# Kernel optimization log

Hardware: AMD Instinct MI355X
Metric: run time of the kernel (lower is better)

## Reference

```python
import jax, jax.numpy as jnp
import numpy as np

DIM = 2048
DIM_HEAD = 64
HEADS = 16
FF_MULT = 4
ATTN_INNER = DIM_HEAD * HEADS          # 1024
FF_INNER = DIM * FF_MULT               # 8192
FUSED = ATTN_INNER + DIM_HEAD + DIM_HEAD + FF_INNER  # 9344
EPS = 1e-8


def setup_inputs() -> dict:
    key = jax.random.key(0)
    ks = jax.random.split(key, 8)
    b, n = 2, 2048
    x = jax.random.normal(ks[0], (b, n, DIM), dtype=jnp.float32)
    g = jnp.ones((DIM,), dtype=jnp.float32)
    s = DIM ** -0.5
    W_fused = jax.random.normal(ks[1], (DIM, FUSED), dtype=jnp.float32) * s
    b_fused = jnp.zeros((FUSED,), dtype=jnp.float32)
    W_attn = jax.random.normal(ks[2], (ATTN_INNER, DIM), dtype=jnp.float32) * ATTN_INNER ** -0.5
    b_attn = jnp.zeros((DIM,), dtype=jnp.float32)
    W_ff = jax.random.normal(ks[3], (FF_INNER, DIM), dtype=jnp.float32) * FF_INNER ** -0.5
    b_ff = jnp.zeros((DIM,), dtype=jnp.float32)
    return {"x": x, "g": g, "W_fused": W_fused, "b_fused": b_fused,
            "W_attn": W_attn, "b_attn": b_attn, "W_ff": W_ff, "b_ff": b_ff}


def _rotate_half(t):
    # last dim split into 2 halves: (x1, x2) -> (-x2, x1)
    x1, x2 = jnp.split(t, 2, axis=-1)
    return jnp.concatenate((-x2, x1), axis=-1)


def _rotary_pos(n, dtype):
    inv_freq = 1.0 / (10000.0 ** (jnp.arange(0, DIM_HEAD, 2, dtype=dtype) / DIM_HEAD))
    freqs = jnp.arange(n, dtype=dtype)[:, None] * inv_freq[None, :]  # [n, d/2]
    return jnp.concatenate((freqs, freqs), axis=-1)                  # [n, d]


def reference(x, g, W_fused, b_fused, W_attn, b_attn, W_ff, b_ff):
    b, n, _ = x.shape
    # RMSNorm (torch-style: L2 norm scaled by dim^-0.5, clamped)
    norm = jnp.linalg.norm(x, axis=-1, keepdims=True) * (DIM ** -0.5)
    xn = x / jnp.maximum(norm, EPS) * g
    # fused qkv + ff projection
    proj = xn @ W_fused + b_fused
    q, k, v, ff = jnp.split(proj, [ATTN_INNER, ATTN_INNER + DIM_HEAD,
                                   ATTN_INNER + 2 * DIM_HEAD], axis=-1)
    q = q.reshape(b, n, HEADS, DIM_HEAD).transpose(0, 2, 1, 3)  # b h n d
    # rotary
    pos = _rotary_pos(n, x.dtype)                # [n, d]
    cos, sin = jnp.cos(pos), jnp.sin(pos)
    q = q * cos + _rotate_half(q) * sin          # broadcasts over b,h
    k = k * cos + _rotate_half(k) * sin          # [b, n, d]
    q = q * (DIM_HEAD ** -0.5)
    # multi-query attention
    sim = jnp.einsum('bhid,bjd->bhij', q, k)
    causal = jnp.triu(jnp.ones((n, n), dtype=bool), k=1)
    sim = jnp.where(causal, -jnp.finfo(sim.dtype).max, sim)
    attn = jax.nn.softmax(sim, axis=-1)
    out = jnp.einsum('bhij,bjd->bhid', attn, v)
    out = out.transpose(0, 2, 1, 3).reshape(b, n, ATTN_INNER)
    attn_out = out @ W_attn + b_attn
    ff_out = jax.nn.gelu(ff, approximate=False) @ W_ff + b_ff
    return attn_out + ff_out
```

## Files before the change

kernel.cpp:

```cpp
#include <hip/hip_runtime.h>
#include <cstdint>
#include <cstddef>

typedef __bf16 bf16_t;
using bf16x8 = __attribute__((ext_vector_type(8))) __bf16;
using f32x4  = __attribute__((ext_vector_type(4))) float;
using u16x4  = __attribute__((ext_vector_type(4))) unsigned short;

#define DEV __device__ __forceinline__

DEV void gload16(const void* g, void* l) {
  __builtin_amdgcn_global_load_lds((const __attribute__((address_space(1))) void*)g,
                                   (__attribute__((address_space(3))) void*)l, 16, 0, 0);
}

__global__ __launch_bounds__(256) void rope_table_kernel(float* cs) {
  int idx = blockIdx.x * 256 + threadIdx.x;
  if (idx >= 2048 * 64) return;
  int n = idx >> 6, d = idx & 63;
  int i = d & 31;
  float freq = (float)n * powf(10000.0f, -(float)i * (1.0f / 32.0f));
  cs[idx]          = cosf(freq);
  cs[131072 + idx] = sinf(freq);
}

__global__ __launch_bounds__(256) void transpose_cvt_kernel(
    const float* __restrict__ in, bf16_t* __restrict__ out,
    int R, int C, int ostride, int coff)
{
  __shared__ bf16_t T[64][80];
  const int c0 = blockIdx.x * 64, r0 = blockIdx.y * 64;
  const int t = threadIdx.x;
  const int lr = t >> 4;
  const int lc = (t & 15) * 4;
#pragma unroll
  for (int i = 0; i < 4; i++) {
    int r = lr + i * 16;
    float4 v = *(const float4*)(in + (size_t)(r0 + r) * C + c0 + lc);
    T[lc + 0][r] = (bf16_t)v.x;
    T[lc + 1][r] = (bf16_t)v.y;
    T[lc + 2][r] = (bf16_t)v.z;
    T[lc + 3][r] = (bf16_t)v.w;
  }
  __syncthreads();
  const int oc = t >> 2;
  const int rc = (t & 3) * 16;
  bf16_t* dst = out + (size_t)(c0 + oc) * ostride + coff + r0 + rc;
  *(bf16x8*)dst       = *(const bf16x8*)&T[oc][rc];
  *(bf16x8*)(dst + 8) = *(const bf16x8*)&T[oc][rc + 8];
}

__global__ __launch_bounds__(256) void rmsnorm_kernel(
    const float* __restrict__ x, const float* __restrict__ g, bf16_t* __restrict__ xn)
{
  const int rid = blockIdx.x;
  const int t = threadIdx.x;
  const float* xr = x + (size_t)rid * 2048;
  float4 v0 = *(const float4*)(xr + t * 8);
  float4 v1 = *(const float4*)(xr + t * 8 + 4);
  float ss = v0.x*v0.x + v0.y*v0.y + v0.z*v0.z + v0.w*v0.w
           + v1.x*v1.x + v1.y*v1.y + v1.z*v1.z + v1.w*v1.w;
#pragma unroll
  for (int m = 1; m < 64; m <<= 1) ss += __shfl_xor(ss, m);
  __shared__ float red[4];
  if ((t & 63) == 0) red[t >> 6] = ss;
  __syncthreads();
  float tot = red[0] + red[1] + red[2] + red[3];
  float norm = sqrtf(tot * (1.0f / 2048.0f));
  float inv = 1.0f / fmaxf(norm, 1e-8f);
  float4 g0 = *(const float4*)(g + t * 8);
  float4 g1 = *(const float4*)(g + t * 8 + 4);
  bf16x8 o;
  o[0] = (bf16_t)(v0.x * inv * g0.x);
  o[1] = (bf16_t)(v0.y * inv * g0.y);
  o[2] = (bf16_t)(v0.z * inv * g0.z);
  o[3] = (bf16_t)(v0.w * inv * g0.w);
  o[4] = (bf16_t)(v1.x * inv * g1.x);
  o[5] = (bf16_t)(v1.y * inv * g1.y);
  o[6] = (bf16_t)(v1.z * inv * g1.z);
  o[7] = (bf16_t)(v1.w * inv * g1.w);
  *(bf16x8*)(xn + (size_t)rid * 2048 + t * 8) = o;
}

__global__ __launch_bounds__(256) void qkv_rope_kernel(
    const bf16_t* __restrict__ qkv, const float* __restrict__ cs,
    bf16_t* __restrict__ qr, bf16_t* __restrict__ kr, bf16_t* __restrict__ vt)
{
  __shared__ float row[1152];
  const int rid = blockIdx.x;
  const int b = rid >> 11, n = rid & 2047;
  const bf16_t* src = qkv + (size_t)rid * 1152;
  for (int c = threadIdx.x; c < 1152; c += 256) row[c] = (float)src[c];
  __syncthreads();
  const float* cosr = cs + n * 64;
  const float* sinr = cs + 131072 + n * 64;
  for (int c = threadIdx.x; c < 1152; c += 256) {
    if (c < 1024) {
      int d = c & 63;
      float cv = cosr[d], sv = sinr[d];
      float x0 = row[c];
      float xr = (d < 32) ? -row[c + 32] : row[c - 32];
      int hh = c >> 6;
      qr[((size_t)(b * 16 + hh) * 2048 + n) * 64 + d] = (bf16_t)((x0 * cv + xr * sv) * 0.125f);
    } else if (c < 1088) {
      int d = c - 1024;
      float cv = cosr[d], sv = sinr[d];
      float x0 = row[c];
      float xr = (d < 32) ? -row[c + 32] : row[c - 32];
      kr[((size_t)b * 2048 + n) * 64 + d] = (bf16_t)(x0 * cv + xr * sv);
    } else {
      int d = c - 1088;
      vt[((size_t)b * 64 + d) * 2048 + n] = src[c];
    }
  }
}

template <int EPI>
__global__ __launch_bounds__(256, 2) void gemm_kernel(
    const bf16_t* __restrict__ A, const bf16_t* __restrict__ Bt, int K,
    const float* __restrict__ bias0, const float* __restrict__ bias1,
    bf16_t* __restrict__ out_qkv, bf16_t* __restrict__ out_ap,
    float* __restrict__ out_f)
{
  __shared__ bf16_t Ash[128 * 64];
  __shared__ bf16_t Bsh[128 * 64];
  const int tid = threadIdx.x;
  const int w = tid >> 6, lane = tid & 63;
  const int wr = w >> 1, wc = w & 1;
  const int m0 = blockIdx.y * 128, n0 = blockIdx.x * 128;
  const int l15 = lane & 15, g4 = lane >> 4;

  f32x4 acc[4][4];
#pragma unroll
  for (int i = 0; i < 4; i++)
#pragma unroll
    for (int j = 0; j < 4; j++) acc[i][j] = f32x4{0.f, 0.f, 0.f, 0.f};

  for (int ks = 0; ks < K; ks += 64) {
    __syncthreads();
#pragma unroll
    for (int i = 0; i < 4; i++) {
      int slot = w * 256 + i * 64 + lane;
      int row = slot >> 3, ch = slot & 7;
      int gch = ch ^ (row & 7);
      gload16(A + (size_t)(m0 + row) * K + ks + gch * 8, (char*)Ash + (w * 4 + i) * 1024);
    }
#pragma unroll
    for (int i = 0; i < 4; i++) {
      int slot = w * 256 + i * 64 + lane;
      int row = slot >> 3, ch = slot & 7;
      int gch = ch ^ (row & 7);
      gload16(Bt + (size_t)(n0 + row) * K + ks + gch * 8, (char*)Bsh + (w * 4 + i) * 1024);
    }
    __syncthreads();
    const char* Ab = (const char*)Ash;
    const char* Bb = (const char*)Bsh;
#pragma unroll
    for (int kc = 0; kc < 2; kc++) {
      bf16x8 af[4], bfr[4];
#pragma unroll
      for (int mi = 0; mi < 4; mi++) {
        int r = wr * 64 + mi * 16 + l15;
        af[mi] = *(const bf16x8*)(Ab + r * 128 + ((kc * 64 + g4 * 16) ^ ((r & 7) << 4)));
      }
#pragma unroll
      for (int ni = 0; ni < 4; ni++) {
        int r = wc * 64 + ni * 16 + l15;
        bfr[ni] = *(const bf16x8*)(Bb + r * 128 + ((kc * 64 + g4 * 16) ^ ((r & 7) << 4)));
      }
#pragma unroll
      for (int mi = 0; mi < 4; mi++)
#pragma unroll
        for (int ni = 0; ni < 4; ni++)
          acc[mi][ni] = __builtin_amdgcn_mfma_f32_16x16x32_bf16(af[mi], bfr[ni], acc[mi][ni], 0, 0, 0);
    }
  }

#pragma unroll
  for (int mi = 0; mi < 4; mi++) {
    const int rb = m0 + wr * 64 + mi * 16 + g4 * 4;
#pragma unroll
    for (int ni = 0; ni < 4; ni++) {
      const int c = n0 + wc * 64 + ni * 16 + l15;
      if (EPI == 0) {
        const float bz = bias0[c];
        if (n0 < 1152) {
#pragma unroll
          for (int j = 0; j < 4; j++)
            out_qkv[(size_t)(rb + j) * 1152 + c] = (bf16_t)(acc[mi][ni][j] + bz);
        } else {
#pragma unroll
          for (int j = 0; j < 4; j++) {
            float v = acc[mi][ni][j] + bz;
            float ge = 0.5f * v * (1.0f + erff(v * 0.70710678118f));
            out_ap[(size_t)(rb + j) * 9216 + (c - 128)] = (bf16_t)ge;
          }
        }
      } else {
        const float bz = bias0[c] + bias1[c];
#pragma unroll
        for (int j = 0; j < 4; j++)
          out_f[(size_t)(rb + j) * 2048 + c] = acc[mi][ni][j] + bz;
      }
    }
  }
}

__global__ __launch_bounds__(64) void attn_kernel(
    const bf16_t* __restrict__ qr, const bf16_t* __restrict__ kr,
    const bf16_t* __restrict__ vt, bf16_t* __restrict__ Ap)
{
  __shared__ bf16_t Ksh[64 * 64];
  __shared__ bf16_t Vsh[64 * 64];
  __shared__ bf16_t Psh[32 * 64];
  const int lane = threadIdx.x;
  const int l15 = lane & 15, g4 = lane >> 4;
  const int qt = blockIdx.x, bh = blockIdx.y;
  const int b = bh >> 4, h = bh & 15;
  const int q0 = qt * 32;

  bf16x8 bq[2][2];
  const bf16_t* qbase = qr + ((size_t)bh * 2048 + q0) * 64;
#pragma unroll
  for (int qi = 0; qi < 2; qi++)
#pragma unroll
    for (int kc = 0; kc < 2; kc++)
      bq[qi][kc] = *(const bf16x8*)(qbase + (qi * 16 + l15) * 64 + kc * 32 + g4 * 8);

  const bf16_t* kb = kr + (size_t)b * 2048 * 64;
  const bf16_t* vb = vt + (size_t)b * 64 * 2048;

  f32x4 acc_o[2][4];
#pragma unroll
  for (int i = 0; i < 2; i++)
#pragma unroll
    for (int j = 0; j < 4; j++) acc_o[i][j] = f32x4{0.f, 0.f, 0.f, 0.f};
  float m_run[2] = {-1e30f, -1e30f};
  float l_run[2] = {0.f, 0.f};
  const int tlast = (q0 + 31) >> 6;

  for (int t = 0; t <= tlast; ++t) {
    const int kv0 = t * 64;
#pragma unroll
    for (int i = 0; i < 8; i++) {
      int slot = i * 64 + lane;
      int row = slot >> 3, ch = slot & 7;
      int gch = ch ^ (row & 7);
      gload16(kb + (size_t)(kv0 + row) * 64 + gch * 8, (char*)Ksh + i * 1024);
    }
#pragma unroll
    for (int i = 0; i < 8; i++) {
      int slot = i * 64 + lane;
      int row = slot >> 3, ch = slot & 7;
      int gch = ch ^ (row & 7);
      gload16(vb + (size_t)row * 2048 + kv0 + gch * 8, (char*)Vsh + i * 1024);
    }
    __syncthreads();

    f32x4 st[4][2];
#pragma unroll
    for (int i = 0; i < 4; i++)
#pragma unroll
      for (int j = 0; j < 2; j++) st[i][j] = f32x4{0.f, 0.f, 0.f, 0.f};
    const char* Kb8 = (const char*)Ksh;
#pragma unroll
    for (int kc = 0; kc < 2; kc++) {
      bf16x8 ak[4];
#pragma unroll
      for (int ni = 0; ni < 4; ni++) {
        int r = ni * 16 + l15;
        ak[ni] = *(const bf16x8*)(Kb8 + r * 128 + ((kc * 64 + g4 * 16) ^ ((r & 7) << 4)));
      }
#pragma unroll
      for (int ni = 0; ni < 4; ni++)
#pragma unroll
        for (int qi = 0; qi < 2; qi++)
          st[ni][qi] = __builtin_amdgcn_mfma_f32_16x16x32_bf16(ak[ni], bq[qi][kc], st[ni][qi], 0, 0, 0);
    }

    if (t == tlast) {
#pragma unroll
      for (int ni = 0; ni < 4; ni++)
#pragma unroll
        for (int qi = 0; qi < 2; qi++)
#pragma unroll
          for (int j = 0; j < 4; j++) {
            int kv = kv0 + ni * 16 + g4 * 4 + j;
            int q  = q0 + qi * 16 + l15;
            if (kv > q) st[ni][qi][j] = -1e30f;
          }
    }

    float sc[2];
#pragma unroll
    for (int qi = 0; qi < 2; qi++) {
      float vm = -1e30f;
#pragma unroll
      for (int ni = 0; ni < 4; ni++)
#pragma unroll
        for (int j = 0; j < 4; j++) vm = fmaxf(vm, st[ni][qi][j]);
      vm = fmaxf(vm, __shfl_xor(vm, 16));
      vm = fmaxf(vm, __shfl_xor(vm, 32));
      float mn = fmaxf(m_run[qi], vm);
      sc[qi] = __expf(m_run[qi] - mn);
      float ps = 0.f;
#pragma unroll
      for (int ni = 0; ni < 4; ni++)
#pragma unroll
        for (int j = 0; j < 4; j++) {
          float p = __expf(st[ni][qi][j] - mn);
          st[ni][qi][j] = p;
          ps += p;
        }
      l_run[qi] = l_run[qi] * sc[qi] + ps;
      m_run[qi] = mn;
    }

#pragma unroll
    for (int mi = 0; mi < 2; mi++)
#pragma unroll
      for (int j = 0; j < 4; j++) {
        float f = __shfl(sc[mi], g4 * 4 + j);
#pragma unroll
        for (int nd = 0; nd < 4; nd++) acc_o[mi][nd][j] *= f;
      }

#pragma unroll
    for (int ni = 0; ni < 4; ni++)
#pragma unroll
      for (int qi = 0; qi < 2; qi++) {
        int q = qi * 16 + l15;
        int kv = ni * 16 + g4 * 4;
        u16x4 pw;
#pragma unroll
        for (int j = 0; j < 4; j++) {
          bf16_t pv = (bf16_t)st[ni][qi][j];
          pw[j] = __builtin_bit_cast(unsigned short, pv);
        }
        *(u16x4*)((char*)Psh + q * 128 + ((kv * 2) ^ ((q & 7) << 4))) = pw;
      }
    __syncthreads();

    const char* Pb8 = (const char*)Psh;
    const char* Vb8 = (const char*)Vsh;
#pragma unroll
    for (int kc = 0; kc < 2; kc++) {
      bf16x8 apf[2], bvf[4];
#pragma unroll
      for (int mi = 0; mi < 2; mi++) {
        int r = mi * 16 + l15;
        apf[mi] = *(const bf16x8*)(Pb8 + r * 128 + ((kc * 64 + g4 * 16) ^ ((r & 7) << 4)));
      }
#pragma unroll
      for (int nd = 0; nd < 4; nd++) {
        int r = nd * 16 + l15;
        bvf[nd] = *(const bf16x8*)(Vb8 + r * 128 + ((kc * 64 + g4 * 16) ^ ((r & 7) << 4)));
      }
#pragma unroll
      for (int mi = 0; mi < 2; mi++)
#pragma unroll
        for (int nd = 0; nd < 4; nd++)
          acc_o[mi][nd] = __builtin_amdgcn_mfma_f32_16x16x32_bf16(apf[mi], bvf[nd], acc_o[mi][nd], 0, 0, 0);
    }
    __syncthreads();
  }

#pragma unroll
  for (int qi = 0; qi < 2; qi++) {
    float l = l_run[qi];
    l += __shfl_xor(l, 16);
    l += __shfl_xor(l, 32);
    l_run[qi] = l;
  }
#pragma unroll
  for (int mi = 0; mi < 2; mi++)
#pragma unroll
    for (int j = 0; j < 4; j++) {
      float linv = 1.0f / __shfl(l_run[mi], g4 * 4 + j);
      int r = q0 + mi * 16 + g4 * 4 + j;
      bf16_t* orow = Ap + (size_t)(b * 2048 + r) * 9216 + h * 64;
#pragma unroll
      for (int nd = 0; nd < 4; nd++)
        orow[nd * 16 + l15] = (bf16_t)(acc_o[mi][nd][j] * linv);
    }
}

extern "C" void kernel_launch(void* const* d_in, const int* in_sizes, int n_in,
                              void* d_out, int out_size, void* d_ws, size_t ws_size,
                              hipStream_t stream)
{
  const float* x       = (const float*)d_in[0];
  const float* g       = (const float*)d_in[1];
  const float* W_fused = (const float*)d_in[2];
  const float* b_fused = (const float*)d_in[3];
  const float* W_attn  = (const float*)d_in[4];
  const float* b_attn  = (const float*)d_in[5];
  const float* W_ff    = (const float*)d_in[6];
  const float* b_ff    = (const float*)d_in[7];
  float* out = (float*)d_out;
  char* ws = (char*)d_ws;

  bf16_t* Wf_t = (bf16_t*)(ws + 0);
  bf16_t* Wc_t = (bf16_t*)(ws + 38273024);
  bf16_t* xn   = (bf16_t*)(ws + 76021760);
  bf16_t* qkv  = (bf16_t*)(ws + 92798976);
  bf16_t* Ap   = (bf16_t*)(ws + 102236160);
  bf16_t* qr   = (bf16_t*)(ws + 177733632);
  bf16_t* kr   = (bf16_t*)(ws + 186122240);
  bf16_t* vt   = (bf16_t*)(ws + 186646528);
  float*  cs   = (float*)(ws + 187170816);

  rope_table_kernel<<<512, 256, 0, stream>>>(cs);
  transpose_cvt_kernel<<<dim3(146, 32), 256, 0, stream>>>(W_fused, Wf_t, 2048, 9344, 2048, 0);
  transpose_cvt_kernel<<<dim3(32, 16),  256, 0, stream>>>(W_attn,  Wc_t, 1024, 2048, 9216, 0);
  transpose_cvt_kernel<<<dim3(32, 128), 256, 0, stream>>>(W_ff,    Wc_t, 8192, 2048, 9216, 1024);
  rmsnorm_kernel<<<4096, 256, 0, stream>>>(x, g, xn);
  gemm_kernel<0><<<dim3(73, 32), 256, 0, stream>>>(xn, Wf_t, 2048, b_fused, nullptr, qkv, Ap, nullptr);
  qkv_rope_kernel<<<4096, 256, 0, stream>>>(qkv, cs, qr, kr, vt);
  attn_kernel<<<dim3(64, 32), 64, 0, stream>>>(qr, kr, vt, Ap);
  gemm_kernel<1><<<dim3(16, 32), 256, 0, stream>>>(Ap, Wc_t, 9216, b_attn, b_ff, nullptr, nullptr, out);
}
```

Baseline: 544.1 us.

## Use 256x256 8-wave GEMM with double-buffered LDS, split-K and reduce

```diff
diff --git a/kernel.cpp b/kernel.cpp
--- a/kernel.cpp
+++ b/kernel.cpp
@@ -13,6 +13,7 @@
   __builtin_amdgcn_global_load_lds((const __attribute__((address_space(1))) void*)g,
                                    (__attribute__((address_space(3))) void*)l, 16, 0, 0);
 }
+DEV int imin(int a, int b) { return a < b ? a : b; }
 
 __global__ __launch_bounds__(256) void rope_table_kernel(float* cs) {
   int idx = blockIdx.x * 256 + threadIdx.x;
@@ -116,94 +117,160 @@
 }
 
 template <int EPI>
-__global__ __launch_bounds__(256, 2) void gemm_kernel(
-    const bf16_t* __restrict__ A, const bf16_t* __restrict__ Bt, int K,
-    const float* __restrict__ bias0, const float* __restrict__ bias1,
+__global__ __launch_bounds__(512, 2) void gemm8p_kernel(
+    const bf16_t* __restrict__ A, const bf16_t* __restrict__ Bt,
+    int strideA, int strideB, int NmaxB, int NT,
+    const float* __restrict__ bias0,
     bf16_t* __restrict__ out_qkv, bf16_t* __restrict__ out_ap,
-    float* __restrict__ out_f)
-{
-  __shared__ bf16_t Ash[128 * 64];
-  __shared__ bf16_t Bsh[128 * 64];
-  const int tid = threadIdx.x;
-  const int w = tid >> 6, lane = tid & 63;
-  const int wr = w >> 1, wc = w & 1;
-  const int m0 = blockIdx.y * 128, n0 = blockIdx.x * 128;
-  const int l15 = lane & 15, g4 = lane >> 4;
-
-  f32x4 acc[4][4];
-#pragma unroll
-  for (int i = 0; i < 4; i++)
+    float* __restrict__ partial)
+{
+  __shared__ bf16_t AB[4][16384];
+  const int tid  = threadIdx.x;
+  const int w    = tid >> 6, lane = tid & 63;
+  const int wm   = w >> 2, wn = w & 3;
+  const int l15  = lane & 15, g4 = lane >> 4;
+
+  const int nwg = gridDim.x;
+  const int wg  = (blockIdx.x & 7) * (nwg >> 3) + (blockIdx.x >> 3);
+  int z = 0, mt, nt;
+  if (EPI == 0) { mt = wg & 15; nt = wg >> 4; }
+  else          { z = wg >> 7; mt = wg & 15; nt = (wg >> 4) & 7; }
+  const int m0 = mt * 256, n0 = nt * 256;
+  const int k0 = z * (NT * 64);
+
+  const bf16_t* Atile = A  + (size_t)m0 * strideA + k0;
+  const bf16_t* Btile = Bt + (size_t)n0 * strideB + k0;
+  const int rbmax = NmaxB - 1 - n0;
+
+  f32x4 acc[8][4];
+#pragma unroll
+  for (int i = 0; i < 8; i++)
 #pragma unroll
     for (int j = 0; j < 4; j++) acc[i][j] = f32x4{0.f, 0.f, 0.f, 0.f};
 
-  for (int ks = 0; ks < K; ks += 64) {
-    __syncthreads();
-#pragma unroll
-    for (int i = 0; i < 4; i++) {
-      int slot = w * 256 + i * 64 + lane;
-      int row = slot >> 3, ch = slot & 7;
-      int gch = ch ^ (row & 7);
-      gload16(A + (size_t)(m0 + row) * K + ks + gch * 8, (char*)Ash + (w * 4 + i) * 1024);
-    }
-#pragma unroll
-    for (int i = 0; i < 4; i++) {
-      int slot = w * 256 + i * 64 + lane;
-      int row = slot >> 3, ch = slot & 7;
-      int gch = ch ^ (row & 7);
-      gload16(Bt + (size_t)(n0 + row) * K + ks + gch * 8, (char*)Bsh + (w * 4 + i) * 1024);
-    }
-    __syncthreads();
-    const char* Ab = (const char*)Ash;
-    const char* Bb = (const char*)Bsh;
-#pragma unroll
-    for (int kc = 0; kc < 2; kc++) {
-      bf16x8 af[4], bfr[4];
+  auto STAGE = [&](int s) {
+    if (s >= 4 * NT) return;
+    const int kts = s >> 2, u = s & 3, buf = kts & 1;
+    const int kk = kts * 64;
+    if (u < 2) {
+      char* ldsT = (char*)AB[buf];
+#pragma unroll
+      for (int i = 0; i < 2; i++) {
+        int slot = u * 1024 + i * 512 + tid;
+        int row = slot >> 3, ks = slot & 7;
+        gload16(Atile + (size_t)row * strideA + kk + ((ks ^ (row & 7)) << 3),
+                ldsT + slot * 16);
+      }
+    } else {
+      char* ldsT = (char*)AB[2 + buf];
+#pragma unroll
+      for (int i = 0; i < 2; i++) {
+        int slot = (u - 2) * 1024 + i * 512 + tid;
+        int row = slot >> 3, ks = slot & 7;
+        int rg = imin(row, rbmax);
+        gload16(Btile + (size_t)rg * strideB + kk + ((ks ^ (row & 7)) << 3),
+                ldsT + slot * 16);
+      }
+    }
+  };
+
+#pragma unroll
+  for (int u = 0; u < 4; ++u) STAGE(u);
+  asm volatile("s_waitcnt vmcnt(0)" ::: "memory");
+  __builtin_amdgcn_s_barrier();
+
+  for (int kt = 0; kt < NT; ++kt) {
+    const int buf = kt & 1;
+    const char* Ab = (const char*)AB[buf];
+    const char* Bb = (const char*)AB[2 + buf];
+#pragma unroll
+    for (int q = 0; q < 4; ++q) {
+      const int mh = q & 1, nh = q >> 1;
+      if (q == 0) {
+#pragma unroll
+        for (int u = 0; u < 4; ++u) STAGE(4 * (kt + 1) + u);
+      }
+      bf16x8 af[4][2], bfr[2][2];
 #pragma unroll
       for (int mi = 0; mi < 4; mi++) {
-        int r = wr * 64 + mi * 16 + l15;
-        af[mi] = *(const bf16x8*)(Ab + r * 128 + ((kc * 64 + g4 * 16) ^ ((r & 7) << 4)));
-      }
-#pragma unroll
-      for (int ni = 0; ni < 4; ni++) {
-        int r = wc * 64 + ni * 16 + l15;
-        bfr[ni] = *(const bf16x8*)(Bb + r * 128 + ((kc * 64 + g4 * 16) ^ ((r & 7) << 4)));
-      }
+        const int r = wm * 128 + mh * 64 + mi * 16 + l15;
+#pragma unroll
+        for (int kc = 0; kc < 2; kc++)
+          af[mi][kc] = *(const bf16x8*)(Ab + r * 128 + (((kc * 4 + g4) ^ (r & 7)) << 4));
+      }
+#pragma unroll
+      for (int ni = 0; ni < 2; ni++) {
+        const int r = wn * 64 + nh * 32 + ni * 16 + l15;
+#pragma unroll
+        for (int kc = 0; kc < 2; kc++)
+          bfr[ni][kc] = *(const bf16x8*)(Bb + r * 128 + (((kc * 4 + g4) ^ (r & 7)) << 4));
+      }
+      __builtin_amdgcn_sched_barrier(0);
+      __builtin_amdgcn_s_barrier();
+      __builtin_amdgcn_s_setprio(1);
 #pragma unroll
       for (int mi = 0; mi < 4; mi++)
 #pragma unroll
-        for (int ni = 0; ni < 4; ni++)
-          acc[mi][ni] = __builtin_amdgcn_mfma_f32_16x16x32_bf16(af[mi], bfr[ni], acc[mi][ni], 0, 0, 0);
-    }
-  }
-
-#pragma unroll
-  for (int mi = 0; mi < 4; mi++) {
-    const int rb = m0 + wr * 64 + mi * 16 + g4 * 4;
-#pragma unroll
-    for (int ni = 0; ni < 4; ni++) {
-      const int c = n0 + wc * 64 + ni * 16 + l15;
+        for (int ni = 0; ni < 2; ni++)
+#pragma unroll
+          for (int kc = 0; kc < 2; kc++)
+            acc[mh * 4 + mi][nh * 2 + ni] =
+              __builtin_amdgcn_mfma_f32_16x16x32_bf16(af[mi][kc], bfr[ni][kc],
+                                                      acc[mh * 4 + mi][nh * 2 + ni], 0, 0, 0);
+      __builtin_amdgcn_s_setprio(0);
+      if (q == 3) asm volatile("s_waitcnt vmcnt(0)" ::: "memory");
+      __builtin_amdgcn_s_barrier();
+    }
+  }
+
+#pragma unroll
+  for (int mi8 = 0; mi8 < 8; mi8++) {
+    const int rb = m0 + wm * 128 + (mi8 >> 2) * 64 + (mi8 & 3) * 16 + g4 * 4;
+#pragma unroll
+    for (int ni4 = 0; ni4 < 4; ni4++) {
+      const int c = n0 + wn * 64 + (ni4 >> 1) * 32 + (ni4 & 1) * 16 + l15;
       if (EPI == 0) {
-        const float bz = bias0[c];
-        if (n0 < 1152) {
+        if (c < 1152) {
+          const float bz = bias0[c];
 #pragma unroll
           for (int j = 0; j < 4; j++)
-            out_qkv[(size_t)(rb + j) * 1152 + c] = (bf16_t)(acc[mi][ni][j] + bz);
-        } else {
+            out_qkv[(size_t)(rb + j) * 1152 + c] = (bf16_t)(acc[mi8][ni4][j] + bz);
+        } else if (c < 9344) {
+          const float bz = bias0[c];
 #pragma unroll
           for (int j = 0; j < 4; j++) {
-            float v = acc[mi][ni][j] + bz;
+            float v = acc[mi8][ni4][j] + bz;
             float ge = 0.5f * v * (1.0f + erff(v * 0.70710678118f));
             out_ap[(size_t)(rb + j) * 9216 + (c - 128)] = (bf16_t)ge;
           }
         }
       } else {
-        const float bz = bias0[c] + bias1[c];
+        float* pz = partial + (size_t)z * (4096 * 2048);
 #pragma unroll
         for (int j = 0; j < 4; j++)
-          out_f[(size_t)(rb + j) * 2048 + c] = acc[mi][ni][j] + bz;
-      }
-    }
-  }
+          pz[(size_t)(rb + j) * 2048 + c] = acc[mi8][ni4][j];
+      }
+    }
+  }
+}
+
+__global__ __launch_bounds__(256) void reduce_kernel(
+    const float* __restrict__ p0, const float* __restrict__ p1,
+    const float* __restrict__ ba, const float* __restrict__ bf,
+    float* __restrict__ out)
+{
+  const size_t e = ((size_t)blockIdx.x * 256 + threadIdx.x) * 4;
+  const int c = (int)(e & 2047);
+  float4 a = *(const float4*)(p0 + e);
+  float4 b = *(const float4*)(p1 + e);
+  float4 x = *(const float4*)(ba + c);
+  float4 y = *(const float4*)(bf + c);
+  float4 o;
+  o.x = a.x + b.x + x.x + y.x;
+  o.y = a.y + b.y + x.y + y.y;
+  o.z = a.z + b.z + x.z + y.z;
+  o.w = a.w + b.w + x.w + y.w;
+  *(float4*)(out + e) = o;
 }
 
 __global__ __launch_bounds__(64) void attn_kernel(
@@ -401,22 +468,26 @@
   char* ws = (char*)d_ws;
 
   bf16_t* Wf_t = (bf16_t*)(ws + 0);
-  bf16_t* Wc_t = (bf16_t*)(ws + 38273024);
-  bf16_t* xn   = (bf16_t*)(ws + 76021760);
-  bf16_t* qkv  = (bf16_t*)(ws + 92798976);
-  bf16_t* Ap   = (bf16_t*)(ws + 102236160);
-  bf16_t* qr   = (bf16_t*)(ws + 177733632);
-  bf16_t* kr   = (bf16_t*)(ws + 186122240);
-  bf16_t* vt   = (bf16_t*)(ws + 186646528);
-  float*  cs   = (float*)(ws + 187170816);
+  bf16_t* xn   = (bf16_t*)(ws + 38273024);
+  bf16_t* qkv  = (bf16_t*)(ws + 55050240);
+  bf16_t* qr   = (bf16_t*)(ws + 64487424);
+  bf16_t* kr   = (bf16_t*)(ws + 72876032);
+  bf16_t* vt   = (bf16_t*)(ws + 73400320);
+  float*  cs   = (float*)(ws + 73924608);
+  float* part  = (float*)(ws + 0);
+  bf16_t* Wc_t = (bf16_t*)(ws + 74973184);
+  bf16_t* Ap   = (bf16_t*)(ws + 112721920);
 
   rope_table_kernel<<<512, 256, 0, stream>>>(cs);
   transpose_cvt_kernel<<<dim3(146, 32), 256, 0, stream>>>(W_fused, Wf_t, 2048, 9344, 2048, 0);
   transpose_cvt_kernel<<<dim3(32, 16),  256, 0, stream>>>(W_attn,  Wc_t, 1024, 2048, 9216, 0);
   transpose_cvt_kernel<<<dim3(32, 128), 256, 0, stream>>>(W_ff,    Wc_t, 8192, 2048, 9216, 1024);
   rmsnorm_kernel<<<4096, 256, 0, stream>>>(x, g, xn);
-  gemm_kernel<0><<<dim3(73, 32), 256, 0, stream>>>(xn, Wf_t, 2048, b_fused, nullptr, qkv, Ap, nullptr);
+  gemm8p_kernel<0><<<592, 512, 0, stream>>>(xn, Wf_t, 2048, 2048, 9344, 32,
+                                            b_fused, qkv, Ap, nullptr);
   qkv_rope_kernel<<<4096, 256, 0, stream>>>(qkv, cs, qr, kr, vt);
   attn_kernel<<<dim3(64, 32), 64, 0, stream>>>(qr, kr, vt, Ap);
-  gemm_kernel<1><<<dim3(16, 32), 256, 0, stream>>>(Ap, Wc_t, 9216, b_attn, b_ff, nullptr, nullptr, out);
-}
+  gemm8p_kernel<2><<<256, 512, 0, stream>>>(Ap, Wc_t, 9216, 9216, 2048, 72,
+                                            nullptr, nullptr, nullptr, part);
+  reduce_kernel<<<8192, 256, 0, stream>>>(part, part + 8388608, b_attn, b_ff, out);
+}
```

After: 608.7 us. 1.12x slower.
